# Optimization experiments

Hardware: AMD Instinct MI355X
Metric: run time of the kernel (lower is better)

## Reference

```python
import jax, jax.numpy as jnp
import numpy as np
from jax import lax

N, CH, H, W = 2, 64, 156, 156
RED, CS, NH = 4, 144, 4
C = CH // RED                                   # 16 = match-embedding dim
L = H * W                                       # 24336 = 169 * CS -> padding = 0
K = L // CS                                     # 169 chunks per hash round
HB = min(L // CS + (L // CS) % 2, 128)          # 128 hash buckets


def _conv2d(x, w):
    return lax.conv_general_dilated(x, w, (1, 1), ((1, 1), (1, 1)),
                                    dimension_numbers=('NCHW', 'OIHW', 'NCHW'))


def _adj(t):
    # concat each bucket with its previous/next bucket along the key axis
    return jnp.concatenate([t, jnp.roll(t, 1, axis=2), jnp.roll(t, -1, axis=2)], axis=3)


def setup_inputs() -> dict:
    key = jax.random.key(0)
    k = jax.random.split(key, 7)
    return {
        'x': jax.random.normal(k[0], (N, CH, H, W), jnp.float32),
        'w_match': jax.random.normal(k[1], (C, CH, 3, 3), jnp.float32) * 0.05,
        'w_assembly': jax.random.normal(k[2], (CH, CH, 3, 3), jnp.float32) * 0.05,
        'w_fc_conv': jax.random.normal(k[3], (CH, CH, 3, 3), jnp.float32) * 0.05,
        'fc_w1': jax.random.normal(k[4], (CS, CH), jnp.float32) * 0.05,
        'fc_b1': jnp.zeros((CS,), jnp.float32),
        'fc_w2': jax.random.normal(k[5], (CS, CS), jnp.float32) * 0.05,
        'fc_b2': jnp.zeros((CS,), jnp.float32),
        'rotations': jax.random.normal(k[6], (C, NH, HB), jnp.float32),
    }


def reference(x, w_match, w_assembly, w_fc_conv, fc_w1, fc_b1, fc_w2, fc_b2, rotations):
    x_embed = _conv2d(x, w_match).reshape(N, C, L).transpose(0, 2, 1)      # (N,L,C)
    y_embed = _conv2d(x, w_assembly).reshape(N, CH, L).transpose(0, 2, 1)  # (N,L,CH)
    fc_embed = _conv2d(x, w_fc_conv).reshape(N, CH, L).transpose(0, 2, 1)  # (N,L,CH)

    # SBLSH hashing (hash codes are detached in the original; argmax blocks grads)
    rotated = jnp.einsum('btf,fhi->bhti', x_embed, rotations)              # (N,NH,L,HB)
    codes = jnp.argmax(rotated, axis=-1) + (jnp.arange(NH) * HB)[None, :, None]
    codes = codes.reshape(N, NH * L)
    indices = jnp.argsort(codes, axis=-1)
    undo_sort = jnp.argsort(indices, axis=-1)
    mod_idx = indices % L
    gather = lambda v: jnp.take_along_axis(v, mod_idx[:, :, None], axis=1)

    x_b = gather(x_embed).reshape(N, NH, K, CS, C)
    y_b = gather(y_embed).reshape(N, NH, K, CS, CH)
    f_b = gather(fc_embed).reshape(N, NH, K, CS, CH)

    x_match = x_b / jnp.maximum(jnp.linalg.norm(x_b, axis=-1, keepdims=True), 5e-5)
    x_match, y_b, f_b = _adj(x_match), _adj(y_b), _adj(f_b)                # key axis -> 3*CS

    h = jax.nn.relu(jnp.einsum('...e,oe->...o', f_b, fc_w1) + fc_b1)
    fc_raw = (jnp.einsum('...e,oe->...o', h, fc_w2) + fc_b2).swapaxes(-1, -2)  # (N,NH,K,CS,3CS)

    raw = jnp.einsum('bhkie,bhkje->bhkij', x_b, x_match) + fc_raw          # (N,NH,K,CS,3CS)
    bucket_score = jax.scipy.special.logsumexp(raw, axis=-1, keepdims=True)
    score = jnp.exp(raw - bucket_score)
    ret = jnp.einsum('bhkij,bhkje->bhkie', score, y_b).reshape(N, NH * L, CH)
    bs = bucket_score.reshape(N, NH * L)

    ret = jnp.take_along_axis(ret, undo_sort[:, :, None], axis=1).reshape(N, NH, L, CH)
    bs = jnp.take_along_axis(bs, undo_sort, axis=1).reshape(N, NH, L, 1)
    probs = jax.nn.softmax(bs, axis=1)                                     # mix hash rounds
    out = jnp.sum(ret * probs, axis=1)                                     # (N,L,CH)
    return out.transpose(0, 2, 1).reshape(N, CH, H, W) + x                 # res_scale = 1
```

## Files before the change

kernel.cpp:

```cpp
#include <hip/hip_runtime.h>

typedef unsigned short u16;
typedef unsigned int   u32;

#define N_ 2
#define CH_ 64
#define H_ 156
#define W_ 156
#define L_ (H_*W_)
#define C_ 16
#define CS_ 144
#define NH_ 4
#define K_ (L_/CS_)
#define HB_ 128
#define M_ (NH_*L_)
#define NBINS 512
#define SORT_BLK 1024
#define NBLK ((M_+SORT_BLK-1)/SORT_BLK)
#define TS 16
#define NTX ((W_+TS-1)/TS)
#define NTY ((H_+TS-1)/TS)
#define CB_ 70
#define RSTR_ (18*CB_)

__device__ __forceinline__ u16 f2bf(float f) {
  union { float f; u32 u; } v; v.f = f;
  u32 r = (v.u + 0x7fffu + ((v.u >> 16) & 1u)) >> 16;
  return (u16)r;
}
__device__ __forceinline__ float bf2f(u16 u) {
  union { u32 u; float f; } v; v.u = ((u32)u) << 16;
  return v.f;
}

typedef __attribute__((ext_vector_type(4))) short short4b;
typedef __attribute__((ext_vector_type(8))) short short8b;
typedef __attribute__((ext_vector_type(4))) float floatx4;

__device__ __forceinline__ short8b pack8(short4b lo, short4b hi) {
  short8b r;
  r[0]=lo[0]; r[1]=lo[1]; r[2]=lo[2]; r[3]=lo[3];
  r[4]=hi[0]; r[5]=hi[1]; r[6]=hi[2]; r[7]=hi[3];
  return r;
}

__device__ __forceinline__ floatx4 mfma32(short8b a, short8b b, floatx4 c) {
  return __builtin_amdgcn_mfma_f32_16x16x32_bf16(a, b, c, 0, 0, 0);
}

__global__ __launch_bounds__(256) void conv_xe_kernel(
    const float* __restrict__ x, const float* __restrict__ wm,
    float* __restrict__ xe)
{
  __shared__ float xs[4][6][18];
  int ct = blockIdx.x % 10, rt = blockIdx.x / 10;
  int b = blockIdx.y;
  int x0 = ct*16, y0 = rt*4;
  int tid = threadIdx.x;
  int px = tid & 63;
  int col = px & 15, row = px >> 4;
  int og = __builtin_amdgcn_readfirstlane(tid >> 6);
  const float* xb = x + (size_t)b*CH_*L_;
  const float* wg = wm + (size_t)og*4*CH_*9;

  float acc[4] = {0.f, 0.f, 0.f, 0.f};
  for (int c0 = 0; c0 < CH_; c0 += 4) {
    __syncthreads();
    for (int i = tid; i < 4*6*18; i += 256) {
      int cc = i / 108, r = i - cc*108;
      int ly = r / 18, lx = r - ly*18;
      int gy = y0 + ly - 1, gx = x0 + lx - 1;
      float v = (gy>=0 && gy<H_ && gx>=0 && gx<W_) ? xb[(size_t)(c0+cc)*L_ + (size_t)gy*W_ + gx] : 0.f;
      xs[cc][ly][lx] = v;
    }
    __syncthreads();
    #pragma unroll
    for (int cc = 0; cc < 4; ++cc) {
      float in[9];
      #pragma unroll
      for (int ky = 0; ky < 3; ++ky)
        #pragma unroll
        for (int kx = 0; kx < 3; ++kx)
          in[ky*3+kx] = xs[cc][row+ky][col+kx];
      const float* wc = wg + (size_t)(c0+cc)*9;
      #pragma unroll
      for (int oo = 0; oo < 4; ++oo) {
        const float* wo = wc + (size_t)oo*CH_*9;
        #pragma unroll
        for (int t = 0; t < 9; ++t) acc[oo] += in[t]*wo[t];
      }
    }
  }
  int gx = x0 + col, gy = y0 + row;
  if (gx < W_) {
    int p = gy*W_ + gx;
    *(float4*)(xe + ((size_t)b*L_+p)*C_ + og*4) = make_float4(acc[0],acc[1],acc[2],acc[3]);
  }
}

__global__ __launch_bounds__(256) void conv_mfma_kernel(
    const float* __restrict__ x, const u16* __restrict__ wpk,
    u16* __restrict__ yeb, u16* __restrict__ feb)
{
  __shared__ u16 xs[6*RSTR_];
  int ct = blockIdx.x % 10, rt = blockIdx.x / 10;
  int b = blockIdx.y;
  int x0 = ct*16, y0 = rt*4;
  int tid = threadIdx.x;
  const float* xb = x + (size_t)b*CH_*L_;

  for (int idx = tid; idx < 64*108; idx += 256) {
    int c = idx / 108, rc = idx - c*108;
    int row = rc / 18, col = rc - row*18;
    int gy = y0 + row - 1, gx = x0 + col - 1;
    float v = (gy>=0 && gy<H_ && gx>=0 && gx<W_) ? xb[(size_t)c*L_ + (size_t)gy*W_ + gx] : 0.f;
    xs[row*RSTR_ + col*CB_ + c] = f2bf(v);
  }
  __syncthreads();

  int wave = tid >> 6, lane = tid & 63;
  int lg = lane >> 4, li = lane & 15;

  floatx4 acc[2][4];
  #pragma unroll
  for (int j = 0; j < 2; ++j)
    #pragma unroll
    for (int pr = 0; pr < 4; ++pr) acc[j][pr] = (floatx4)(0.f);

  #pragma unroll
  for (int tap = 0; tap < 9; ++tap) {
    int ky = tap / 3, kx = tap - ky*3;
    short8b A[2][2];
    #pragma unroll
    for (int j = 0; j < 2; ++j) {
      int ot = wave + j*4;
      const u16* wr = wpk + (((size_t)ot*9 + tap)*16 + li)*64;
      A[j][0] = pack8(*(const short4b*)(wr + lg*4),      *(const short4b*)(wr + 16 + lg*4));
      A[j][1] = pack8(*(const short4b*)(wr + 32 + lg*4), *(const short4b*)(wr + 48 + lg*4));
    }
    #pragma unroll
    for (int pr = 0; pr < 4; ++pr) {
      const u16* bp = xs + (pr+ky)*RSTR_ + (li+kx)*CB_;
      short8b B0 = pack8(*(const short4b*)(bp + lg*4),      *(const short4b*)(bp + 16 + lg*4));
      short8b B1 = pack8(*(const short4b*)(bp + 32 + lg*4), *(const short4b*)(bp + 48 + lg*4));
      acc[0][pr] = mfma32(A[0][0], B0, acc[0][pr]);
      acc[0][pr] = mfma32(A[0][1], B1, acc[0][pr]);
      acc[1][pr] = mfma32(A[1][0], B0, acc[1][pr]);
      acc[1][pr] = mfma32(A[1][1], B1, acc[1][pr]);
    }
  }

  int px = x0 + li;
  if (px < W_) {
    #pragma unroll
    for (int pr = 0; pr < 4; ++pr) {
      int p = (y0+pr)*W_ + px;
      short4b v0, v1;
      #pragma unroll
      for (int r = 0; r < 4; ++r) {
        v0[r] = (short)f2bf(acc[0][pr][r]);
        v1[r] = (short)f2bf(acc[1][pr][r]);
      }
      *(short4b*)(yeb + ((size_t)b*L_+p)*64 + wave*16 + lg*4) = v0;
      *(short4b*)(feb + ((size_t)b*L_+p)*64 + wave*16 + lg*4) = v1;
    }
  }
}

__global__ __launch_bounds__(256) void hash_kernel(
    const float* __restrict__ xe, const float* __restrict__ rot,
    u16* __restrict__ xnb, int* __restrict__ codes)
{
  __shared__ float rl[NH_*HB_*C_];
  int tid = threadIdx.x;
  int b = blockIdx.y;
  for (int idx = tid; idx < NH_*HB_*C_; idx += 256) {
    int f = idx & 15; int hi = idx >> 4; int h = hi >> 7; int i = hi & 127;
    rl[idx] = rot[((size_t)f*NH_ + h)*HB_ + i];
  }
  __syncthreads();
  int t = blockIdx.x * 256 + tid;
  if (t >= L_) return;
  float xr[C_];
  float ss = 0.f;
  #pragma unroll
  for (int f = 0; f < C_; ++f) { xr[f] = xe[((size_t)b*L_ + t)*C_ + f]; ss += xr[f]*xr[f]; }
  float inv = 1.f / fmaxf(sqrtf(ss), 5e-5f);
  u32 w[8];
  #pragma unroll
  for (int q = 0; q < 8; ++q)
    w[q] = (u32)f2bf(xr[2*q]*inv) | ((u32)f2bf(xr[2*q+1]*inv) << 16);
  uint4* d = (uint4*)(xnb + ((size_t)b*L_ + t)*C_);
  d[0] = make_uint4(w[0],w[1],w[2],w[3]);
  d[1] = make_uint4(w[4],w[5],w[6],w[7]);
  #pragma unroll
  for (int h = 0; h < NH_; ++h) {
    float best = -1e30f; int bi = 0;
    #pragma unroll 2
    for (int i = 0; i < HB_; ++i) {
      const float4* rp = (const float4*)(rl + (h*HB_ + i)*C_);
      float4 r0 = rp[0], r1 = rp[1], r2 = rp[2], r3 = rp[3];
      float v = 0.f;
      v += xr[0]*r0.x;  v += xr[1]*r0.y;  v += xr[2]*r0.z;  v += xr[3]*r0.w;
      v += xr[4]*r1.x;  v += xr[5]*r1.y;  v += xr[6]*r1.z;  v += xr[7]*r1.w;
      v += xr[8]*r2.x;  v += xr[9]*r2.y;  v += xr[10]*r2.z; v += xr[11]*r2.w;
      v += xr[12]*r3.x; v += xr[13]*r3.y; v += xr[14]*r3.z; v += xr[15]*r3.w;
      if (v > best) { best = v; bi = i; }
    }
    codes[(size_t)b*M_ + h*L_ + t] = bi + h*HB_;
  }
}

__global__ __launch_bounds__(256) void prep_w_kernel(
    const float* __restrict__ w1, const float* __restrict__ w2,
    const float* __restrict__ wa, const float* __restrict__ wf,
    u16* __restrict__ w1b, u16* __restrict__ w2b, u16* __restrict__ wpk)
{
  int i = blockIdx.x*256 + threadIdx.x;
  if (i < CS_*CH_)  w1b[i] = f2bf(w1[i]);
  if (i < CS_*CS_)  w2b[i] = f2bf(w2[i]);
  if (i < 8*9*16*64) {
    int ot = i / (9*16*64); int r = i - ot*(9*16*64);
    int tap = r / (16*64);  int r2 = r - tap*(16*64);
    int o = r2 >> 6, c = r2 & 63;
    const float* src = (ot < 4) ? wa : wf;
    int og = (ot & 3)*16 + o;
    wpk[i] = f2bf(src[((size_t)og*64 + c)*9 + tap]);
  }
}

__global__ __launch_bounds__(256) void fc_mfma_kernel(
    const u16* __restrict__ feb, const u16* __restrict__ w1b, const float* __restrict__ b1,
    const u16* __restrict__ w2b, const float* __restrict__ b2, u16* __restrict__ fc2b)
{
  int wid = blockIdx.x*4 + (threadIdx.x >> 6);
  if (wid >= 2*(L_/16)) return;
  int b = wid / (L_/16);
  int p0 = (wid - b*(L_/16)) * 16;
  int lane = threadIdx.x & 63;
  int lg = lane >> 4, li = lane & 15;

  const u16* fr = feb + ((size_t)b*L_ + p0 + li)*CH_;
  short8b feB[2];
  #pragma unroll
  for (int ks = 0; ks < 2; ++ks)
    feB[ks] = pack8(*(const short4b*)(fr + ks*32 + lg*4),
                    *(const short4b*)(fr + ks*32 + 16 + lg*4));

  short4b hq[9];
  #pragma unroll
  for (int s = 0; s < 9; ++s) {
    const u16* wr = w1b + (size_t)(s*16 + li)*CH_ + lg*4;
    short8b a0 = pack8(*(const short4b*)(wr),      *(const short4b*)(wr + 16));
    short8b a1 = pack8(*(const short4b*)(wr + 32), *(const short4b*)(wr + 48));
    floatx4 acc = mfma32(a0, feB[0], (floatx4)(0.f));
    acc = mfma32(a1, feB[1], acc);
    float4 bb = *(const float4*)(b1 + s*16 + lg*4);
    short4b hv;
    hv[0] = (short)f2bf(fmaxf(acc[0] + bb.x, 0.f));
    hv[1] = (short)f2bf(fmaxf(acc[1] + bb.y, 0.f));
    hv[2] = (short)f2bf(fmaxf(acc[2] + bb.z, 0.f));
    hv[3] = (short)f2bf(fmaxf(acc[3] + bb.w, 0.f));
    hq[s] = hv;
  }
  short4b zero4; zero4[0]=0; zero4[1]=0; zero4[2]=0; zero4[3]=0;
  short8b hB[5];
  #pragma unroll
  for (int ks = 0; ks < 4; ++ks) hB[ks] = pack8(hq[2*ks], hq[2*ks+1]);
  hB[4] = pack8(hq[8], zero4);

  u16* orow = fc2b + ((size_t)b*L_ + p0 + li)*CS_;
  #pragma unroll
  for (int s2 = 0; s2 < 9; ++s2) {
    const u16* wr = w2b + (size_t)(s2*16 + li)*CS_;
    floatx4 acc = (floatx4)(0.f);
    #pragma unroll
    for (int ks = 0; ks < 5; ++ks) {
      short4b lo = *(const short4b*)(wr + ks*32 + lg*4);
      short4b hi = (ks < 4) ? *(const short4b*)(wr + ks*32 + 16 + lg*4) : zero4;
      acc = mfma32(pack8(lo, hi), hB[ks], acc);
    }
    float4 bb = *(const float4*)(b2 + s2*16 + lg*4);
    short4b ov;
    ov[0] = (short)f2bf(acc[0] + bb.x);
    ov[1] = (short)f2bf(acc[1] + bb.y);
    ov[2] = (short)f2bf(acc[2] + bb.z);
    ov[3] = (short)f2bf(acc[3] + bb.w);
    *(short4b*)(orow + s2*16 + lg*4) = ov;
  }
}

__global__ __launch_bounds__(256) void hist_kernel(
    const int* __restrict__ codes, int* __restrict__ hist)
{
  __shared__ int lh[NBINS];
  int eb = blockIdx.x, b = blockIdx.y;
  for (int i = threadIdx.x; i < NBINS; i += 256) lh[i] = 0;
  __syncthreads();
  int base = eb * SORT_BLK;
  int end = min(base + SORT_BLK, M_);
  for (int i = base + threadIdx.x; i < end; i += 256)
    atomicAdd(&lh[codes[(size_t)b*M_ + i]], 1);
  __syncthreads();
  for (int i = threadIdx.x; i < NBINS; i += 256)
    hist[((size_t)b*NBLK + eb)*NBINS + i] = lh[i];
}

__global__ __launch_bounds__(NBINS) void prefix_kernel(
    const int* __restrict__ hist, int* __restrict__ blockoff, int* __restrict__ bin_start)
{
  int b = blockIdx.x;
  int c = threadIdx.x;
  int run = 0;
  for (int eb = 0; eb < NBLK; ++eb) {
    size_t idx = ((size_t)b*NBLK + eb)*NBINS + c;
    int v = hist[idx];
    blockoff[idx] = run;
    run += v;
  }
  __shared__ int tot[NBINS];
  tot[c] = run;
  __syncthreads();
  if (c == 0) {
    int s = 0;
    for (int i = 0; i < NBINS; ++i) { int v = tot[i]; tot[i] = s; s += v; }
  }
  __syncthreads();
  bin_start[b*NBINS + c] = tot[c];
}

__global__ __launch_bounds__(64) void scatter_kernel(
    const int* __restrict__ codes, const int* __restrict__ bin_start,
    const int* __restrict__ blockoff, int* __restrict__ idx_sorted)
{
  __shared__ int off[NBINS];
  __shared__ int lc[SORT_BLK];
  int eb = blockIdx.x, b = blockIdx.y;
  for (int i = threadIdx.x; i < NBINS; i += 64)
    off[i] = bin_start[b*NBINS + i] + blockoff[((size_t)b*NBLK + eb)*NBINS + i];
  int base = eb * SORT_BLK;
  int end = min(base + SORT_BLK, M_);
  for (int i = base + threadIdx.x; i < end; i += 64)
    lc[i - base] = codes[(size_t)b*M_ + i];
  __syncthreads();
  if (threadIdx.x == 0) {
    int n = end - base;
    for (int i = 0; i < n; ++i) {
      int c = lc[i];
      int p = off[c]++;
      idx_sorted[(size_t)b*M_ + p] = base + i;
    }
  }
}

__global__ __launch_bounds__(192) void bucket_kernel(
    const float* __restrict__ xe, const u16* __restrict__ xnb,
    const u16* __restrict__ yeb, const u16* __restrict__ fc2b,
    const int* __restrict__ idx_sorted,
    float* __restrict__ retbuf, float* __restrict__ bsbuf)
{
  __shared__ u16 k_lds[432*16];
  __shared__ u16 v_lds[64*436 + 16];
  __shared__ int tj[432];
  __shared__ int o_own[144];

  int flat = blockIdx.x;
  int sid = (flat & 7)*169 + (flat >> 3);
  int k  = sid % K_;
  int hb = sid / K_;
  int h = hb & 3, b = hb >> 2;
  int tid = threadIdx.x;
  int kprev = (k + K_ - 1) % K_, knext = (k + 1) % K_;
  const int* iss = idx_sorted + (size_t)b*M_ + (size_t)h*K_*CS_;
  const u16* xnbb = xnb + (size_t)b*L_*C_;

  for (int j = tid; j < 3*CS_; j += 192) {
    int jb = j / CS_, ji = j - jb*CS_;
    int kj = jb==0 ? k : (jb==1 ? kprev : knext);
    int orig = iss[kj*CS_ + ji];
    int t = orig % L_;
    tj[j] = t;
    if (jb == 0) o_own[ji] = orig;
    const uint4* s = (const uint4*)(xnbb + (size_t)t*C_);
    uint4* d = (uint4*)(k_lds + j*16);
    d[0] = s[0]; d[1] = s[1];
  }
  __syncthreads();

  const u16* yb = yeb + (size_t)b*L_*64;
  for (int idx = tid; idx < 216*64; idx += 192) {
    int p2 = idx >> 6, ch = idx & 63;
    u32 lo = yb[(size_t)tj[2*p2]*64 + ch];
    u32 hi = yb[(size_t)tj[2*p2+1]*64 + ch];
    ((u32*)v_lds)[ch*218 + p2] = lo | (hi << 16);
  }

  int wave = tid >> 6, lane = tid & 63;
  int lg = lane >> 4, li = lane & 15;
  int wq0 = wave * 48;

  short4b zero4; zero4[0]=0; zero4[1]=0; zero4[2]=0; zero4[3]=0;

  short8b qb[3];
  const float* xeb_ = xe + (size_t)b*L_*C_;
  #pragma unroll
  for (int n = 0; n < 3; ++n) {
    int t = tj[wq0 + n*16 + li];
    const float* q = xeb_ + (size_t)t*C_ + lg*4;
    short4b v;
    v[0] = (short)f2bf(q[0]); v[1] = (short)f2bf(q[1]);
    v[2] = (short)f2bf(q[2]); v[3] = (short)f2bf(q[3]);
    qb[n] = pack8(v, zero4);
  }

  const u16* fb = fc2b + (size_t)b*L_*CS_;
  u16 bnx[2][3][4];
  #pragma unroll
  for (int s2 = 0; s2 < 2; ++s2)
    #pragma unroll
    for (int r = 0; r < 4; ++r) {
      int t = tj[s2*16 + lg*4 + r];
      #pragma unroll
      for (int n = 0; n < 3; ++n)
        bnx[s2][n][r] = fb[(size_t)t*CS_ + wq0 + n*16 + li];
    }
  __syncthreads();

  floatx4 oacc[4][3];
  #pragma unroll
  for (int cg = 0; cg < 4; ++cg)
    #pragma unroll
    for (int n = 0; n < 3; ++n)
      oacc[cg][n] = (floatx4)(0.f);
  float mrun[3] = {-1e30f,-1e30f,-1e30f};
  float lsum[3] = {0.f,0.f,0.f};

  for (int p = 0; p < 13; ++p) {
    int t0 = 2*p, t1 = 2*p+1;
    short8b ak0 = pack8(*(const short4b*)(k_lds + (size_t)(t0*16 + li)*16 + lg*4), zero4);
    short8b ak1 = pack8(*(const short4b*)(k_lds + (size_t)(t1*16 + li)*16 + lg*4), zero4);
    floatx4 s0[3], s1[3];
    #pragma unroll
    for (int n = 0; n < 3; ++n) {
      s0[n] = mfma32(ak0, qb[n], (floatx4)(0.f));
      s1[n] = mfma32(ak1, qb[n], (floatx4)(0.f));
    }
    float bias0[3][4], bias1[3][4];
    #pragma unroll
    for (int n = 0; n < 3; ++n)
      #pragma unroll
      for (int r = 0; r < 4; ++r) {
        bias0[n][r] = bf2f(bnx[0][n][r]);
        bias1[n][r] = bf2f(bnx[1][n][r]);
      }
    if (p < 12) {
      #pragma unroll
      for (int s2 = 0; s2 < 2; ++s2)
        #pragma unroll
        for (int r = 0; r < 4; ++r) {
          int t = tj[(2*p+2+s2)*16 + lg*4 + r];
          #pragma unroll
          for (int n = 0; n < 3; ++n)
            bnx[s2][n][r] = fb[(size_t)t*CS_ + wq0 + n*16 + li];
        }
    } else {
      #pragma unroll
      for (int r = 0; r < 4; ++r) {
        int t = tj[26*16 + lg*4 + r];
        #pragma unroll
        for (int n = 0; n < 3; ++n)
          bnx[0][n][r] = fb[(size_t)t*CS_ + wq0 + n*16 + li];
      }
    }

    short8b pb[3];
    #pragma unroll
    for (int n = 0; n < 3; ++n) {
      float a0[4], a1[4];
      #pragma unroll
      for (int r = 0; r < 4; ++r) { a0[r] = s0[n][r] + bias0[n][r]; a1[r] = s1[n][r] + bias1[n][r]; }
      float tmax = fmaxf(fmaxf(fmaxf(a0[0],a0[1]), fmaxf(a0[2],a0[3])),
                         fmaxf(fmaxf(a1[0],a1[1]), fmaxf(a1[2],a1[3])));
      tmax = fmaxf(tmax, __shfl_xor(tmax, 16));
      tmax = fmaxf(tmax, __shfl_xor(tmax, 32));
      if (__any(tmax > mrun[n] + 8.f)) {
        float mn = fmaxf(mrun[n], tmax);
        float sc = __expf(mrun[n] - mn);
        lsum[n] *= sc;
        #pragma unroll
        for (int cg = 0; cg < 4; ++cg) {
          oacc[cg][n][0] *= sc; oacc[cg][n][1] *= sc;
          oacc[cg][n][2] *= sc; oacc[cg][n][3] *= sc;
        }
        mrun[n] = mn;
      }
      float pv0[4], pv1[4];
      float ls = 0.f;
      #pragma unroll
      for (int r = 0; r < 4; ++r) {
        pv0[r] = __expf(a0[r] - mrun[n]);
        pv1[r] = __expf(a1[r] - mrun[n]);
        ls += pv0[r] + pv1[r];
      }
      lsum[n] += ls;
      short4b plo, phi;
      #pragma unroll
      for (int r = 0; r < 4; ++r) {
        plo[r] = (short)f2bf(pv0[r]);
        phi[r] = (short)f2bf(pv1[r]);
      }
      pb[n] = pack8(plo, phi);
    }
    #pragma unroll
    for (int cg = 0; cg < 4; ++cg) {
      const u16* vr = v_lds + (size_t)(cg*16 + li)*436 + p*32 + lg*4;
      short8b av = pack8(*(const short4b*)vr, *(const short4b*)(vr + 16));
      #pragma unroll
      for (int n = 0; n < 3; ++n)
        oacc[cg][n] = mfma32(av, pb[n], oacc[cg][n]);
    }
  }

  {
    short8b ak0 = pack8(*(const short4b*)(k_lds + (size_t)(26*16 + li)*16 + lg*4), zero4);
    floatx4 s0[3];
    #pragma unroll
    for (int n = 0; n < 3; ++n)
      s0[n] = mfma32(ak0, qb[n], (floatx4)(0.f));
    short8b pb[3];
    #pragma unroll
    for (int n = 0; n < 3; ++n) {
      float a0[4];
      #pragma unroll
      for (int r = 0; r < 4; ++r) a0[r] = s0[n][r] + bf2f(bnx[0][n][r]);
      float tmax = fmaxf(fmaxf(a0[0],a0[1]), fmaxf(a0[2],a0[3]));
      tmax = fmaxf(tmax, __shfl_xor(tmax, 16));
      tmax = fmaxf(tmax, __shfl_xor(tmax, 32));
      if (__any(tmax > mrun[n] + 8.f)) {
        float mn = fmaxf(mrun[n], tmax);
        float sc = __expf(mrun[n] - mn);
        lsum[n] *= sc;
        #pragma unroll
        for (int cg = 0; cg < 4; ++cg) {
          oacc[cg][n][0] *= sc; oacc[cg][n][1] *= sc;
          oacc[cg][n][2] *= sc; oacc[cg][n][3] *= sc;
        }
        mrun[n] = mn;
      }
      float ls = 0.f;
      short4b plo;
      #pragma unroll
      for (int r = 0; r < 4; ++r) {
        float pv = __expf(a0[r] - mrun[n]);
        ls += pv;
        plo[r] = (short)f2bf(pv);
      }
      lsum[n] += ls;
      pb[n] = pack8(plo, zero4);
    }
    #pragma unroll
    for (int cg = 0; cg < 4; ++cg) {
      const u16* vr = v_lds + (size_t)(cg*16 + li)*436 + 416 + lg*4;
      short8b av = pack8(*(const short4b*)vr, zero4);
      #pragma unroll
      for (int n = 0; n < 3; ++n)
        oacc[cg][n] = mfma32(av, pb[n], oacc[cg][n]);
    }
  }

  float bs[3], inv[3];
  #pragma unroll
  for (int n = 0; n < 3; ++n) {
    float ls = lsum[n];
    ls += __shfl_xor(ls, 16);
    ls += __shfl_xor(ls, 32);
    inv[n] = 1.f / ls;
    bs[n] = mrun[n] + logf(ls);
  }
  if (lane < 16) {
    #pragma unroll
    for (int n = 0; n < 3; ++n)
      bsbuf[(size_t)b*M_ + o_own[wq0 + n*16 + lane]] = bs[n];
  }
  __syncthreads();
  float* o_lds = (float*)v_lds;
  #pragma unroll
  for (int cg = 0; cg < 4; ++cg)
    #pragma unroll
    for (int n = 0; n < 3; ++n)
      #pragma unroll
      for (int r = 0; r < 4; ++r)
        o_lds[(size_t)(wq0 + n*16 + li)*68 + cg*16 + lg*4 + r] = oacc[cg][n][r] * inv[n];
  __syncthreads();
  float* rb = retbuf + (size_t)b*M_*64;
  for (int rr = tid >> 4; rr < 144; rr += 12) {
    int c4 = (tid & 15)*4;
    const float* src = o_lds + (size_t)rr*68 + c4;
    float4 v = make_float4(src[0], src[1], src[2], src[3]);
    *(float4*)(rb + (size_t)o_own[rr]*64 + c4) = v;
  }
}

__global__ __launch_bounds__(256) void combine_kernel(
    const float* __restrict__ retbuf, const float* __restrict__ bsbuf,
    const float* __restrict__ x, float* __restrict__ out)
{
  __shared__ float s[64][65];
  __shared__ float prob[NH_][64];
  int b = blockIdx.y;
  int p0 = blockIdx.x * 64;
  int tid = threadIdx.x;
  if (tid < 64) {
    int p = min(p0 + tid, L_-1);
    float bs0 = bsbuf[(size_t)b*M_ + 0*L_ + p];
    float bs1 = bsbuf[(size_t)b*M_ + 1*L_ + p];
    float bs2 = bsbuf[(size_t)b*M_ + 2*L_ + p];
    float bs3 = bsbuf[(size_t)b*M_ + 3*L_ + p];
    float mx = fmaxf(fmaxf(bs0,bs1), fmaxf(bs2,bs3));
    float e0 = __expf(bs0-mx), e1 = __expf(bs1-mx), e2 = __expf(bs2-mx), e3 = __expf(bs3-mx);
    float inv = 1.f / (e0+e1+e2+e3);
    prob[0][tid] = e0*inv; prob[1][tid] = e1*inv;
    prob[2][tid] = e2*inv; prob[3][tid] = e3*inv;
  }
  __syncthreads();
  for (int i = tid; i < 64*64; i += 256) {
    int pp = i >> 6, c = i & 63;
    int p = min(p0 + pp, L_-1);
    float v = 0.f;
    #pragma unroll
    for (int h = 0; h < NH_; ++h)
      v += retbuf[(((size_t)b*NH_ + h)*L_ + p)*CH_ + c] * prob[h][pp];
    s[c][pp] = v;
  }
  __syncthreads();
  for (int i = tid; i < 64*64; i += 256) {
    int pp = i & 63, cc = i >> 6;
    int p = p0 + pp;
    if (p < L_) {
      size_t gi = ((size_t)b*CH_ + cc)*L_ + p;
      out[gi] = s[cc][pp] + x[gi];
    }
  }
}

extern "C" void kernel_launch(void* const* d_in, const int* in_sizes, int n_in,
                              void* d_out, int out_size, void* d_ws, size_t ws_size,
                              hipStream_t stream) {
  const float* x   = (const float*)d_in[0];
  const float* wm  = (const float*)d_in[1];
  const float* wa  = (const float*)d_in[2];
  const float* wf  = (const float*)d_in[3];
  const float* fw1 = (const float*)d_in[4];
  const float* fb1 = (const float*)d_in[5];
  const float* fw2 = (const float*)d_in[6];
  const float* fb2 = (const float*)d_in[7];
  const float* rot = (const float*)d_in[8];
  float* out = (float*)d_out;

  char* p = (char*)d_ws;
  auto alloc = [&](size_t bytes) { char* r = p; p += (bytes + 255) & ~(size_t)255; return r; };
  float* xe      = (float*)alloc(sizeof(float)*(size_t)N_*L_*C_);
  u16*   xnb     = (u16*)  alloc(sizeof(u16)*(size_t)N_*L_*C_);
  u16*   yeb     = (u16*)  alloc(sizeof(u16)*(size_t)N_*L_*CH_);
  u16*   feb     = (u16*)  alloc(sizeof(u16)*(size_t)N_*L_*CH_);
  u16*   fc2b    = (u16*)  alloc(sizeof(u16)*(size_t)N_*L_*CS_);
  float* retbuf  = (float*)alloc(sizeof(float)*(size_t)N_*M_*CH_);
  float* bsbuf   = (float*)alloc(sizeof(float)*(size_t)N_*M_);
  int* codes     = (int*)alloc(sizeof(int)*(size_t)N_*M_);
  int* idx_sorted= (int*)alloc(sizeof(int)*(size_t)N_*M_);
  int* hist      = (int*)alloc(sizeof(int)*(size_t)N_*NBLK*NBINS);
  int* blockoff  = (int*)alloc(sizeof(int)*(size_t)N_*NBLK*NBINS);
  int* bin_start = (int*)alloc(sizeof(int)*(size_t)N_*NBINS);
  u16* w1b       = (u16*)alloc(sizeof(u16)*(size_t)CS_*CH_);
  u16* w2b       = (u16*)alloc(sizeof(u16)*(size_t)CS_*CS_);
  u16* wpk       = (u16*)alloc(sizeof(u16)*(size_t)8*9*16*64);

  prep_w_kernel<<<dim3((8*9*16*64 + 255)/256), 256, 0, stream>>>(fw1, fw2, wa, wf, w1b, w2b, wpk);
  conv_xe_kernel<<<dim3(10*39, N_), 256, 0, stream>>>(x, wm, xe);
  conv_mfma_kernel<<<dim3(10*39, N_), 256, 0, stream>>>(x, wpk, yeb, feb);
  hash_kernel<<<dim3((L_ + 255)/256, N_), 256, 0, stream>>>(xe, rot, xnb, codes);
  {
    int tiles = 2*(L_/16);
    fc_mfma_kernel<<<dim3((tiles + 3)/4), 256, 0, stream>>>(feb, w1b, fb1, w2b, fb2, fc2b);
  }
  {
    dim3 g(NBLK, N_);
    hist_kernel<<<g, 256, 0, stream>>>(codes, hist);
    prefix_kernel<<<dim3(N_), NBINS, 0, stream>>>(hist, blockoff, bin_start);
    scatter_kernel<<<g, 64, 0, stream>>>(codes, bin_start, blockoff, idx_sorted);
  }
  bucket_kernel<<<dim3(K_*NH_*N_), 192, 0, stream>>>(xe, xnb, yeb, fc2b,
                                                     idx_sorted, retbuf, bsbuf);
  combine_kernel<<<dim3((L_ + 63)/64, N_), 256, 0, stream>>>(retbuf, bsbuf, x, out);
}
```

Measured before the change: 432.6 us.

## Halve bucket kernel LDS via two-phase V staging and bf16 retbuf

Result: slower. 468.6 us (+8.3%).

```diff
diff --git a/kernel.cpp b/kernel.cpp
--- a/kernel.cpp
+++ b/kernel.cpp
@@ -357,12 +357,14 @@
     const float* __restrict__ xe, const u16* __restrict__ xnb,
     const u16* __restrict__ yeb, const u16* __restrict__ fc2b,
     const int* __restrict__ idx_sorted,
-    float* __restrict__ retbuf, float* __restrict__ bsbuf)
-{
-  __shared__ u16 k_lds[432*16];
-  __shared__ u16 v_lds[64*436 + 16];
-  __shared__ int tj[432];
-  __shared__ int o_own[144];
+    u16* __restrict__ retbuf, float* __restrict__ bsbuf)
+{
+  __shared__ char smem[45056];
+  u16* k_lds = (u16*)smem;
+  u16* v_lds = (u16*)(smem + 13824);
+  int* tj    = (int*)(smem + 42752);
+  int* o_own = (int*)(smem + 44480);
+  u16* o_lds = (u16*)smem;
 
   int flat = blockIdx.x;
   int sid = (flat & 7)*169 + (flat >> 3);
@@ -388,11 +390,11 @@
   __syncthreads();
 
   const u16* yb = yeb + (size_t)b*L_*64;
-  for (int idx = tid; idx < 216*64; idx += 192) {
+  for (int idx = tid; idx < 112*64; idx += 192) {
     int p2 = idx >> 6, ch = idx & 63;
     u32 lo = yb[(size_t)tj[2*p2]*64 + ch];
     u32 hi = yb[(size_t)tj[2*p2+1]*64 + ch];
-    ((u32*)v_lds)[ch*218 + p2] = lo | (hi << 16);
+    ((u32*)v_lds)[ch*113 + p2] = lo | (hi << 16);
   }
 
   int wave = tid >> 6, lane = tid & 63;
@@ -436,6 +438,17 @@
   float lsum[3] = {0.f,0.f,0.f};
 
   for (int p = 0; p < 13; ++p) {
+    if (p == 7) {
+      __syncthreads();
+      for (int idx = tid; idx < 104*64; idx += 192) {
+        int p2 = idx >> 6, ch = idx & 63;
+        int kk = 224 + 2*p2;
+        u32 lo = yb[(size_t)tj[kk]*64 + ch];
+        u32 hi = yb[(size_t)tj[kk+1]*64 + ch];
+        ((u32*)v_lds)[ch*113 + p2] = lo | (hi << 16);
+      }
+      __syncthreads();
+    }
     int t0 = 2*p, t1 = 2*p+1;
     short8b ak0 = pack8(*(const short4b*)(k_lds + (size_t)(t0*16 + li)*16 + lg*4), zero4);
     short8b ak1 = pack8(*(const short4b*)(k_lds + (size_t)(t1*16 + li)*16 + lg*4), zero4);
@@ -511,14 +524,17 @@
       }
       pb[n] = pack8(plo, phi);
     }
+    int vloc = (p < 7) ? p*32 : (p-7)*32;
+    __builtin_amdgcn_s_setprio(1);
     #pragma unroll
     for (int cg = 0; cg < 4; ++cg) {
-      const u16* vr = v_lds + (size_t)(cg*16 + li)*436 + p*32 + lg*4;
+      const u16* vr = v_lds + (size_t)(cg*16 + li)*226 + vloc + lg*4;
       short8b av = pack8(*(const short4b*)vr, *(const short4b*)(vr + 16));
       #pragma unroll
       for (int n = 0; n < 3; ++n)
         oacc[cg][n] = mfma32(av, pb[n], oacc[cg][n]);
     }
+    __builtin_amdgcn_s_setprio(0);
   }
 
   {
@@ -558,14 +574,16 @@
       lsum[n] += ls;
       pb[n] = pack8(plo, zero4);
     }
+    __builtin_amdgcn_s_setprio(1);
     #pragma unroll
     for (int cg = 0; cg < 4; ++cg) {
-      const u16* vr = v_lds + (size_t)(cg*16 + li)*436 + 416 + lg*4;
+      const u16* vr = v_lds + (size_t)(cg*16 + li)*226 + 192 + lg*4;
       short8b av = pack8(*(const short4b*)vr, zero4);
       #pragma unroll
       for (int n = 0; n < 3; ++n)
         oacc[cg][n] = mfma32(av, pb[n], oacc[cg][n]);
     }
+    __builtin_amdgcn_s_setprio(0);
   }
 
   float bs[3], inv[3];
@@ -583,26 +601,26 @@
       bsbuf[(size_t)b*M_ + o_own[wq0 + n*16 + lane]] = bs[n];
   }
   __syncthreads();
-  float* o_lds = (float*)v_lds;
   #pragma unroll
   for (int cg = 0; cg < 4; ++cg)
     #pragma unroll
-    for (int n = 0; n < 3; ++n)
-      #pragma unroll
-      for (int r = 0; r < 4; ++r)
-        o_lds[(size_t)(wq0 + n*16 + li)*68 + cg*16 + lg*4 + r] = oacc[cg][n][r] * inv[n];
-  __syncthreads();
-  float* rb = retbuf + (size_t)b*M_*64;
+    for (int n = 0; n < 3; ++n) {
+      short4b ov;
+      #pragma unroll
+      for (int r = 0; r < 4; ++r) ov[r] = (short)f2bf(oacc[cg][n][r] * inv[n]);
+      *(short4b*)(o_lds + (size_t)(wq0 + n*16 + li)*72 + cg*16 + lg*4) = ov;
+    }
+  __syncthreads();
+  u16* rbb = retbuf + (size_t)b*M_*64;
   for (int rr = tid >> 4; rr < 144; rr += 12) {
     int c4 = (tid & 15)*4;
-    const float* src = o_lds + (size_t)rr*68 + c4;
-    float4 v = make_float4(src[0], src[1], src[2], src[3]);
-    *(float4*)(rb + (size_t)o_own[rr]*64 + c4) = v;
+    short4b v = *(const short4b*)(o_lds + (size_t)rr*72 + c4);
+    *(short4b*)(rbb + (size_t)o_own[rr]*64 + c4) = v;
   }
 }
 
 __global__ __launch_bounds__(256) void combine_kernel(
-    const float* __restrict__ retbuf, const float* __restrict__ bsbuf,
+    const u16* __restrict__ retbuf, const float* __restrict__ bsbuf,
     const float* __restrict__ x, float* __restrict__ out)
 {
   __shared__ float s[64][65];
@@ -629,7 +647,7 @@
     float v = 0.f;
     #pragma unroll
     for (int h = 0; h < NH_; ++h)
-      v += retbuf[(((size_t)b*NH_ + h)*L_ + p)*CH_ + c] * prob[h][pp];
+      v += bf2f(retbuf[(((size_t)b*NH_ + h)*L_ + p)*CH_ + c]) * prob[h][pp];
     s[c][pp] = v;
   }
   __syncthreads();
@@ -664,7 +682,7 @@
   u16*   yeb     = (u16*)  alloc(sizeof(u16)*(size_t)N_*L_*CH_);
   u16*   feb     = (u16*)  alloc(sizeof(u16)*(size_t)N_*L_*CH_);
   u16*   fc2b    = (u16*)  alloc(sizeof(u16)*(size_t)N_*L_*CS_);
-  float* retbuf  = (float*)alloc(sizeof(float)*(size_t)N_*M_*CH_);
+  u16*   retbuf  = (u16*)  alloc(sizeof(u16)*(size_t)N_*M_*CH_);
   float* bsbuf   = (float*)alloc(sizeof(float)*(size_t)N_*M_);
   int* codes     = (int*)alloc(sizeof(int)*(size_t)N_*M_);
   int* idx_sorted= (int*)alloc(sizeof(int)*(size_t)N_*M_);
```
